# Kernel optimization log

Hardware: AMD Instinct MI355X
Metric: run time of the kernel (lower is better)

Reference implementation:

```python
import jax, jax.numpy as jnp
import numpy as np

B, C, H, W = 4, 128, 128, 128
G, K = 4, 3
P = K * K
STRIDE, PAD, DIL = 1, 1, 1
OFFSET_SCALE = 1.0


def setup_inputs() -> dict:
    key = jax.random.key(0)
    k1, k2, k3, k4 = jax.random.split(key, 4)
    inp = jax.random.normal(k1, (B, C, H, W), jnp.float32)
    # offset / mask linear params (zero-init in source; small random here for a
    # nontrivial sampling pattern -- same math, different param values)
    W_off = jax.random.normal(k2, (C, G * P * 2), jnp.float32) * 0.01
    b_off = jax.random.normal(k3, (G * P * 2,), jnp.float32) * 0.5
    W_mask = jax.random.normal(k4, (C, G * P), jnp.float32) * 0.02
    b_mask = jnp.zeros((G * P,), jnp.float32)
    return {"inp": inp, "W_off": W_off, "b_off": b_off, "W_mask": W_mask, "b_mask": b_mask}


def _dcnv3_core(x, offset, mask):
    # x: (b,h,w,c)  offset: (b,h,w,G*P*2)  mask: (b,h,w,G*P)
    b, h, w, c = x.shape
    gc = c // G
    xp = jnp.pad(x, ((0, 0), (PAD, PAD), (PAD, PAD), (0, 0)))
    H_in, W_in = h + 2 * PAD, w + 2 * PAD
    H_out = (H_in - (DIL * (K - 1) + 1)) // STRIDE + 1
    W_out = (W_in - (DIL * (K - 1) + 1)) // STRIDE + 1
    Q = H_out * W_out

    # reference points, normalized to padded size (matches _get_reference_points)
    base = (DIL * (K - 1)) // 2 + 0.5
    ref_y = (base + jnp.arange(H_out, dtype=jnp.float32) * STRIDE) / H_in
    ref_x = (base + jnp.arange(W_out, dtype=jnp.float32) * STRIDE) / W_in
    ref = jnp.stack(jnp.broadcast_arrays(ref_x[None, :], ref_y[:, None]), -1)  # (Ho,Wo,2) as (x,y)

    # dilation grid (matches _generate_dilation_grids; torch meshgrid flatten is x-major)
    off0 = -((DIL * (K - 1)) // 2)
    ks = off0 + jnp.arange(K, dtype=jnp.float32) * DIL
    gx = jnp.repeat(ks, K) / W_in  # (P,)
    gy = jnp.tile(ks, K) / H_in
    grid = jnp.stack([gx, gy], -1)  # (P,2), identical for every group

    norm = jnp.array([W_in, H_in], jnp.float32)
    loc = (ref[None, :, :, None, None, :]
           + grid[None, None, None, None, :, :] * OFFSET_SCALE
           + offset.reshape(b, H_out, W_out, G, P, 2) * (OFFSET_SCALE / norm))  # (b,Ho,Wo,G,P,2)

    # grid_sample(bilinear, zeros, align_corners=False): pixel = loc*size - 0.5
    px = loc[..., 0] * W_in - 0.5
    py = loc[..., 1] * H_in - 0.5
    x0 = jnp.floor(px); y0 = jnp.floor(py)
    tx = px - x0; ty = py - y0
    x0i = x0.astype(jnp.int32); y0i = y0.astype(jnp.int32)

    xg = xp.reshape(b, H_in * W_in, G, gc)

    def corner(ix, iy, wgt):
        valid = (ix >= 0) & (ix < W_in) & (iy >= 0) & (iy < H_in)
        lin = jnp.clip(iy, 0, H_in - 1) * W_in + jnp.clip(ix, 0, W_in - 1)
        idx = lin.reshape(b, Q, G, P).transpose(0, 1, 3, 2).reshape(b, Q * P, G)
        g = jnp.take_along_axis(xg, idx[..., None], axis=1)  # (b,Q*P,G,gc)
        wv = jnp.where(valid, wgt, 0.0).reshape(b, Q, G, P).transpose(0, 1, 3, 2).reshape(b, Q * P, G, 1)
        return g * wv

    val = (corner(x0i, y0i, (1 - tx) * (1 - ty))
           + corner(x0i + 1, y0i, tx * (1 - ty))
           + corner(x0i, y0i + 1, (1 - tx) * ty)
           + corner(x0i + 1, y0i + 1, tx * ty))  # (b,Q*P,G,gc)

    m = mask.reshape(b, Q, G, P).transpose(0, 1, 3, 2).reshape(b, Q, P, G, 1)
    out = (val.reshape(b, Q, P, G, gc) * m).sum(axis=2)  # (b,Q,G,gc)
    return out.reshape(b, H_out, W_out, G * gc)


def reference(inp, W_off, b_off, W_mask, b_mask):
    b, c, h, w = inp.shape
    x = inp.reshape(b, h, w, c)  # torch .view reinterpretation (faithful to source)
    offset = x @ W_off + b_off  # (b,h,w,G*P*2)
    mask = jax.nn.softmax((x @ W_mask + b_mask).reshape(b, h, w, G, P), axis=-1).reshape(b, h, w, G * P)
    out = _dcnv3_core(x, offset, mask)  # (b,h,w,c)
    return out.reshape(b, c, h, w)
```

## Files before the change

kernel.cpp:

```cpp
#include <hip/hip_runtime.h>


#define NPIX 65536

typedef unsigned int uint;
typedef unsigned short ushort;
typedef __attribute__((ext_vector_type(8))) short short8v;
typedef __attribute__((ext_vector_type(4))) float f32x4;

__device__ __forceinline__ ushort f2bf(float f) {
  uint u = __float_as_uint(f);
  u += 0x7FFFu + ((u >> 16) & 1u);
  return (ushort)(u >> 16);
}
__device__ __forceinline__ uint pkbf(float lo, float hi) {
  return (uint)f2bf(lo) | ((uint)f2bf(hi) << 16);
}
__device__ __forceinline__ float bflo(uint d) { return __uint_as_float(d << 16); }
__device__ __forceinline__ float bfhi(uint d) { return __uint_as_float(d & 0xFFFF0000u); }
__device__ __forceinline__ ushort f2h(float f) {
  union { _Float16 h; ushort u; } cv;
  cv.h = (_Float16)f;
  return cv.u;
}
__device__ __forceinline__ float h2f(ushort u) {
  union { ushort u; _Float16 h; } cv;
  cv.u = u;
  return (float)cv.h;
}

union U8 { uint u[4]; short8v v; };

__global__ __launch_bounds__(256) void dcn_lin_mfma(
    const float* __restrict__ x, const float* __restrict__ Woff,
    const float* __restrict__ boff, const float* __restrict__ Wmask,
    const float* __restrict__ bmask, ushort* __restrict__ ws16,
    ushort* __restrict__ x16) {
  __shared__ uint wt[112 * 68];
  __shared__ float bias_lds[112];
  const int pbase = blockIdx.x << 6;
  const int t = threadIdx.x;

  {
    int n = t, row = 0;
    bool act = true;
    if (t >= 224) act = false;
    else if (t >= 112) { n = t - 112; row = 1; }
    if (act) {
      for (int kp = row; kp < 64; kp += 2) {
        const int k = kp << 1;
        float w0, w1;
        if (n < 72) {
          w0 = Woff[k * 72 + n];        w1 = Woff[k * 72 + 72 + n];
        } else if (n < 108) {
          w0 = Wmask[k * 36 + n - 72];  w1 = Wmask[k * 36 + 36 + n - 72];
        } else {
          w0 = 0.f; w1 = 0.f;
        }
        wt[n * 68 + kp] = pkbf(w0, w1);
      }
    }
    if (t < 112)
      bias_lds[t] = (t < 72) ? boff[t] : (t < 108 ? bmask[t - 72] : 0.f);
  }

  if (x16) {
    const int pix2 = pbase + (t >> 2);
    const int quad = t & 3;
    const float* xp = x + (size_t)pix2 * 128 + (quad << 5);
    const int bb = pix2 >> 14, yx = pix2 & 16383;
    ushort* dst = x16 + ((((size_t)((quad << 2) | bb) << 14) | yx) << 5);
#pragma unroll
    for (int ck = 0; ck < 2; ++ck) {
      const float4 a = *(const float4*)(xp + ck * 16);
      const float4 b4 = *(const float4*)(xp + ck * 16 + 4);
      const float4 c4 = *(const float4*)(xp + ck * 16 + 8);
      const float4 d4 = *(const float4*)(xp + ck * 16 + 12);
      uint4 s0, s1;
      s0.x = pkbf(a.x, a.y);   s0.y = pkbf(a.z, a.w);
      s0.z = pkbf(b4.x, b4.y); s0.w = pkbf(b4.z, b4.w);
      s1.x = pkbf(c4.x, c4.y); s1.y = pkbf(c4.z, c4.w);
      s1.z = pkbf(d4.x, d4.y); s1.w = pkbf(d4.z, d4.w);
      *(uint4*)(dst + ck * 16) = s0;
      *(uint4*)(dst + ck * 16 + 8) = s1;
    }
  }
  __syncthreads();

  const int wv = t >> 6;
  const int lane = t & 63;
  const int lrow = lane & 15;
  const int lhi = lane >> 4;
  const int pixrow = pbase + (wv << 4) + lrow;

  U8 afr[4];
#pragma unroll
  for (int kt = 0; kt < 4; ++kt) {
    const float* ax = x + (size_t)pixrow * 128 + (kt << 5) + (lhi << 3);
    const float4 xa = *(const float4*)ax;
    const float4 xb4 = *(const float4*)(ax + 4);
    afr[kt].u[0] = pkbf(xa.x, xa.y);   afr[kt].u[1] = pkbf(xa.z, xa.w);
    afr[kt].u[2] = pkbf(xb4.x, xb4.y); afr[kt].u[3] = pkbf(xb4.z, xb4.w);
  }

  f32x4 acc[7];
#pragma unroll
  for (int nt = 0; nt < 7; ++nt) {
    const float bv = bias_lds[(nt << 4) + lrow];
    f32x4 a4 = {bv, bv, bv, bv};
#pragma unroll
    for (int kt = 0; kt < 4; ++kt) {
      U8 bfr;
      const uint4 bw =
          *(const uint4*)(wt + ((nt << 4) + lrow) * 68 + (kt << 4) + (lhi << 2));
      bfr.u[0] = bw.x; bfr.u[1] = bw.y; bfr.u[2] = bw.z; bfr.u[3] = bw.w;
      a4 = __builtin_amdgcn_mfma_f32_16x16x32_bf16(afr[kt].v, bfr.v, a4, 0, 0, 0);
    }
    acc[nt] = a4;
  }

  const int rowb = pbase + (wv << 4) + (lhi << 2);
#pragma unroll
  for (int nt = 0; nt < 7; ++nt) {
    const int n = (nt << 4) + lrow;
    if (n < 108) {
      ushort4 hv;
      hv.x = f2h(acc[nt].x);
      hv.y = f2h(acc[nt].y);
      hv.z = f2h(acc[nt].z);
      hv.w = f2h(acc[nt].w);
      *(ushort4*)(ws16 + (size_t)n * NPIX + rowb) = hv;
    }
  }
}

__global__ __launch_bounds__(256) void dcn_samp(
    const ushort* __restrict__ x16, const ushort* __restrict__ ws16,
    float* __restrict__ out) {
  const int g = blockIdx.x & 3;
  const int pg = threadIdx.x >> 2;
  const int sub = threadIdx.x & 3;
  const int q = ((blockIdx.x >> 2) << 6) | pg;
  const int b = q >> 14;
  const int h = (q >> 7) & 127;
  const int w = q & 127;
  const ushort* wsq = ws16 + q;
  const ushort* xg = x16 + (((size_t)((g << 2) | b)) << 19) + (sub << 3);

  float mk9[9];
  {
    float mx = -1e30f;
#pragma unroll
    for (int p = 0; p < 9; ++p) {
      mk9[p] = h2f(wsq[(size_t)(72 + g * 9 + p) * NPIX]);
      mx = fmaxf(mx, mk9[p]);
    }
    float s = 0.f;
#pragma unroll
    for (int p = 0; p < 9; ++p) {
      mk9[p] = __expf(mk9[p] - mx);
      s += mk9[p];
    }
    const float sinv = 1.0f / s;
#pragma unroll
    for (int p = 0; p < 9; ++p) mk9[p] *= sinv;
  }

  float a0 = 0.f, a1 = 0.f, a2 = 0.f, a3 = 0.f;
  float a4 = 0.f, a5 = 0.f, a6 = 0.f, a7 = 0.f;

#pragma unroll
  for (int p = 0; p < 9; ++p) {
    const float offx = h2f(wsq[(size_t)(g * 18 + 2 * p) * NPIX]);
    const float offy = h2f(wsq[(size_t)(g * 18 + 2 * p + 1) * NPIX]);
    const float mk = mk9[p];
    const float px = (float)(w + p / 3) + offx;
    const float py = (float)(h + p % 3) + offy;
    const float fx = floorf(px), fy = floorf(py);
    const float tx = px - fx, ty = py - fy;
    const int x0 = (int)fx - 1, y0 = (int)fy - 1;
    const int x1 = x0 + 1, y1 = y0 + 1;
    const float ax0 = ((unsigned)x0 < 128u) ? (1.f - tx) : 0.f;
    const float ax1 = ((unsigned)x1 < 128u) ? tx : 0.f;
    const float ay0 = ((unsigned)y0 < 128u) ? (mk * (1.f - ty)) : 0.f;
    const float ay1 = ((unsigned)y1 < 128u) ? (mk * ty) : 0.f;
    const float w00 = ax0 * ay0, w10 = ax1 * ay0;
    const float w01 = ax0 * ay1, w11 = ax1 * ay1;
    const int cx0 = min(max(x0, 0), 127), cy0 = min(max(y0, 0), 127);
    const int cx1 = min(max(x1, 0), 127), cy1 = min(max(y1, 0), 127);
    const int o00 = ((cy0 << 7) | cx0) << 5;
    const int o10 = ((cy0 << 7) | cx1) << 5;
    const int o01 = ((cy1 << 7) | cx0) << 5;
    const int o11 = ((cy1 << 7) | cx1) << 5;
    const uint4 d00 = *(const uint4*)(xg + o00);
    const uint4 d10 = *(const uint4*)(xg + o10);
    const uint4 d01 = *(const uint4*)(xg + o01);
    const uint4 d11 = *(const uint4*)(xg + o11);
    a0 = fmaf(w00, bflo(d00.x), fmaf(w10, bflo(d10.x),
         fmaf(w01, bflo(d01.x), fmaf(w11, bflo(d11.x), a0))));
    a1 = fmaf(w00, bfhi(d00.x), fmaf(w10, bfhi(d10.x),
         fmaf(w01, bfhi(d01.x), fmaf(w11, bfhi(d11.x), a1))));
    a2 = fmaf(w00, bflo(d00.y), fmaf(w10, bflo(d10.y),
         fmaf(w01, bflo(d01.y), fmaf(w11, bflo(d11.y), a2))));
    a3 = fmaf(w00, bfhi(d00.y), fmaf(w10, bfhi(d10.y),
         fmaf(w01, bfhi(d01.y), fmaf(w11, bfhi(d11.y), a3))));
    a4 = fmaf(w00, bflo(d00.z), fmaf(w10, bflo(d10.z),
         fmaf(w01, bflo(d01.z), fmaf(w11, bflo(d11.z), a4))));
    a5 = fmaf(w00, bfhi(d00.z), fmaf(w10, bfhi(d10.z),
         fmaf(w01, bfhi(d01.z), fmaf(w11, bfhi(d11.z), a5))));
    a6 = fmaf(w00, bflo(d00.w), fmaf(w10, bflo(d10.w),
         fmaf(w01, bflo(d01.w), fmaf(w11, bflo(d11.w), a6))));
    a7 = fmaf(w00, bfhi(d00.w), fmaf(w10, bfhi(d10.w),
         fmaf(w01, bfhi(d01.w), fmaf(w11, bfhi(d11.w), a7))));
  }

  float* op = out + (size_t)q * 128 + (g << 5) + (sub << 3);
  float4 oa, ob;
  oa.x = a0; oa.y = a1; oa.z = a2; oa.w = a3;
  ob.x = a4; ob.y = a5; ob.z = a6; ob.w = a7;
  *(float4*)op = oa;
  *(float4*)(op + 4) = ob;
}

__global__ __launch_bounds__(256) void dcn_lin(
    const float* __restrict__ x, const float* __restrict__ Woff,
    const float* __restrict__ boff, const float* __restrict__ Wmask,
    const float* __restrict__ bmask, float* __restrict__ ws) {
  const int jg = blockIdx.x >> 8;
  const int pix = ((blockIdx.x & 255) << 8) | threadIdx.x;
  const float* W;
  const float* bias;
  int ldw, obase;
  if (jg == 0) {
    W = Woff; bias = boff; ldw = 72; obase = 0;
  } else if (jg == 1) {
    W = Woff + 36; bias = boff + 36; ldw = 72; obase = 36;
  } else {
    W = Wmask; bias = bmask; ldw = 36; obase = 72;
  }
  float acc[36];
#pragma unroll
  for (int j = 0; j < 36; ++j) acc[j] = bias[j];
  const float* xp = x + (size_t)pix * 128;
  for (int c0 = 0; c0 < 128; c0 += 8) {
    float xr[8];
    *(float4*)(xr) = *(const float4*)(xp + c0);
    *(float4*)(xr + 4) = *(const float4*)(xp + c0 + 4);
#pragma unroll
    for (int cc = 0; cc < 8; ++cc) {
      const float xc = xr[cc];
      const float* wr = W + (size_t)(c0 + cc) * ldw;
#pragma unroll
      for (int j = 0; j < 36; ++j) acc[j] = fmaf(xc, wr[j], acc[j]);
    }
  }
  if (jg == 2) {
#pragma unroll
    for (int g = 0; g < 4; ++g) {
      float mx = acc[g * 9];
#pragma unroll
      for (int p = 1; p < 9; ++p) mx = fmaxf(mx, acc[g * 9 + p]);
      float s = 0.f;
#pragma unroll
      for (int p = 0; p < 9; ++p) {
        acc[g * 9 + p] = __expf(acc[g * 9 + p] - mx);
        s += acc[g * 9 + p];
      }
      const float sinv = 1.0f / s;
#pragma unroll
      for (int p = 0; p < 9; ++p) acc[g * 9 + p] *= sinv;
    }
  }
#pragma unroll
  for (int j = 0; j < 36; ++j) ws[(size_t)(obase + j) * NPIX + pix] = acc[j];
}

__global__ __launch_bounds__(256) void dcn_samp_f32(
    const float* __restrict__ x, const float* __restrict__ ws,
    float* __restrict__ out) {
  const int q = (blockIdx.x << 4) | (threadIdx.x >> 4);
  const int sub = threadIdx.x & 15;
  const int c = sub << 3;
  const int g = sub >> 2;
  const int b = q >> 14;
  const int h = (q >> 7) & 127;
  const int w = q & 127;
  const float* xb = x + ((size_t)b << 21) + c;
  const float* wsq = ws + q;
  float a0 = 0.f, a1 = 0.f, a2 = 0.f, a3 = 0.f;
  float a4 = 0.f, a5 = 0.f, a6 = 0.f, a7 = 0.f;
#pragma unroll
  for (int p = 0; p < 9; ++p) {
    const float offx = wsq[(size_t)(g * 18 + p * 2) * NPIX];
    const float offy = wsq[(size_t)(g * 18 + p * 2 + 1) * NPIX];
    const float mk = wsq[(size_t)(72 + g * 9 + p) * NPIX];
    const float px = (float)(w + p / 3) + offx;
    const float py = (float)(h + p % 3) + offy;
    const float fx = floorf(px), fy = floorf(py);
    const float tx = px - fx, ty = py - fy;
    const int x0 = (int)fx - 1, y0 = (int)fy - 1;
    const int x1 = x0 + 1, y1 = y0 + 1;
    const float ax0 = ((unsigned)x0 < 128u) ? (1.f - tx) : 0.f;
    const float ax1 = ((unsigned)x1 < 128u) ? tx : 0.f;
    const float ay0 = ((unsigned)y0 < 128u) ? (mk * (1.f - ty)) : 0.f;
    const float ay1 = ((unsigned)y1 < 128u) ? (mk * ty) : 0.f;
    const float w00 = ax0 * ay0, w10 = ax1 * ay0;
    const float w01 = ax0 * ay1, w11 = ax1 * ay1;
    const int cx0 = min(max(x0, 0), 127), cy0 = min(max(y0, 0), 127);
    const int cx1 = min(max(x1, 0), 127), cy1 = min(max(y1, 0), 127);
    const int o00 = (cy0 << 14) | (cx0 << 7), o10 = (cy0 << 14) | (cx1 << 7);
    const int o01 = (cy1 << 14) | (cx0 << 7), o11 = (cy1 << 14) | (cx1 << 7);
    const float4 v00a = *(const float4*)(xb + o00);
    const float4 v00b = *(const float4*)(xb + o00 + 4);
    const float4 v10a = *(const float4*)(xb + o10);
    const float4 v10b = *(const float4*)(xb + o10 + 4);
    const float4 v01a = *(const float4*)(xb + o01);
    const float4 v01b = *(const float4*)(xb + o01 + 4);
    const float4 v11a = *(const float4*)(xb + o11);
    const float4 v11b = *(const float4*)(xb + o11 + 4);
    a0 = fmaf(w00, v00a.x, fmaf(w10, v10a.x, fmaf(w01, v01a.x, fmaf(w11, v11a.x, a0))));
    a1 = fmaf(w00, v00a.y, fmaf(w10, v10a.y, fmaf(w01, v01a.y, fmaf(w11, v11a.y, a1))));
    a2 = fmaf(w00, v00a.z, fmaf(w10, v10a.z, fmaf(w01, v01a.z, fmaf(w11, v11a.z, a2))));
    a3 = fmaf(w00, v00a.w, fmaf(w10, v10a.w, fmaf(w01, v01a.w, fmaf(w11, v11a.w, a3))));
    a4 = fmaf(w00, v00b.x, fmaf(w10, v10b.x, fmaf(w01, v01b.x, fmaf(w11, v11b.x, a4))));
    a5 = fmaf(w00, v00b.y, fmaf(w10, v10b.y, fmaf(w01, v01b.y, fmaf(w11, v11b.y, a5))));
    a6 = fmaf(w00, v00b.z, fmaf(w10, v10b.z, fmaf(w01, v01b.z, fmaf(w11, v11b.z, a6))));
    a7 = fmaf(w00, v00b.w, fmaf(w10, v10b.w, fmaf(w01, v01b.w, fmaf(w11, v11b.w, a7))));
  }
  float4 oa, ob;
  oa.x = a0; oa.y = a1; oa.z = a2; oa.w = a3;
  ob.x = a4; ob.y = a5; ob.z = a6; ob.w = a7;
  float* op = out + (size_t)q * 128 + c;
  *(float4*)op = oa;
  *(float4*)(op + 4) = ob;
}

__global__ __launch_bounds__(128) void dcn_fused(
    const float* __restrict__ x, const float* __restrict__ Woff,
    const float* __restrict__ boff, const float* __restrict__ Wmask,
    const float* __restrict__ bmask, float* __restrict__ out) {
  __shared__ float xs[128];
  __shared__ float res[108];
  __shared__ float msk[36];
  const int q = blockIdx.x;
  const int t = threadIdx.x;
  const int b = q >> 14, h = (q >> 7) & 127, w = q & 127;
  xs[t] = x[(size_t)q * 128 + t];
  __syncthreads();
  if (t < 108) {
    float a;
    const float* W;
    int ld;
    if (t < 72) {
      a = boff[t]; W = Woff + t; ld = 72;
    } else {
      a = bmask[t - 72]; W = Wmask + (t - 72); ld = 36;
    }
    for (int cc = 0; cc < 128; ++cc) a = fmaf(xs[cc], W[(size_t)cc * ld], a);
    res[t] = a;
  }
  __syncthreads();
  if (t < 4) {
    float mx = -1e30f;
    for (int p = 0; p < 9; ++p) mx = fmaxf(mx, res[72 + t * 9 + p]);
    float s = 0.f;
    float e[9];
    for (int p = 0; p < 9; ++p) {
      e[p] = __expf(res[72 + t * 9 + p] - mx);
      s += e[p];
    }
    for (int p = 0; p < 9; ++p) msk[t * 9 + p] = e[p] / s;
  }
  __syncthreads();
  const int g = t >> 5;
  const float* xb = x + ((size_t)b << 21) + t;
  float acc = 0.f;
#pragma unroll
  for (int p = 0; p < 9; ++p) {
    const float offx = res[g * 18 + p * 2];
    const float offy = res[g * 18 + p * 2 + 1];
    const float px = (float)(w + p / 3) + offx;
    const float py = (float)(h + p % 3) + offy;
    const float fx = floorf(px), fy = floorf(py);
    const float tx = px - fx, ty = py - fy;
    const int x0 = (int)fx - 1, y0 = (int)fy - 1;
    float sv = 0.f;
#define CORNER1(XI, YI, WT)                                       \
  if ((unsigned)(XI) < 128u && (unsigned)(YI) < 128u)             \
    sv = fmaf((WT), xb[((size_t)(YI) << 14) + ((size_t)(XI) << 7)], sv);
    CORNER1(x0, y0, (1.f - tx) * (1.f - ty))
    CORNER1(x0 + 1, y0, tx * (1.f - ty))
    CORNER1(x0, y0 + 1, (1.f - tx) * ty)
    CORNER1(x0 + 1, y0 + 1, tx * ty)
#undef CORNER1
    acc = fmaf(msk[g * 9 + p], sv, acc);
  }
  out[(size_t)q * 128 + t] = acc;
}

extern "C" void kernel_launch(void* const* d_in, const int* in_sizes, int n_in,
                              void* d_out, int out_size, void* d_ws,
                              size_t ws_size, hipStream_t stream) {
  const float* x = (const float*)d_in[0];
  const float* Woff = (const float*)d_in[1];
  const float* boff = (const float*)d_in[2];
  const float* Wmask = (const float*)d_in[3];
  const float* bmask = (const float*)d_in[4];
  float* out = (float*)d_out;
  const size_t need_ws = (size_t)NPIX * 108 * sizeof(float);
  const size_t need_full = (size_t)NPIX * (128 + 108) * sizeof(ushort);
  if (ws_size >= need_full) {
    ushort* x16 = (ushort*)d_ws;
    ushort* ws16 = (ushort*)d_ws + (size_t)NPIX * 128;
    dcn_lin_mfma<<<1024, 256, 0, stream>>>(x, Woff, boff, Wmask, bmask, ws16,
                                           x16);
    dcn_samp<<<4096, 256, 0, stream>>>(x16, ws16, out);
  } else if (ws_size >= need_ws) {
    float* ws = (float*)d_ws;
    dcn_lin<<<768, 256, 0, stream>>>(x, Woff, boff, Wmask, bmask, ws);
    dcn_samp_f32<<<4096, 256, 0, stream>>>(x, ws, out);
  } else {
    dcn_fused<<<NPIX, 128, 0, stream>>>(x, Woff, boff, Wmask, bmask, out);
  }
}
```

Baseline: 62.05 us.

## Store offset/mask workspace pixel-major with per-group 32-half records

The linear kernel now transposes its MFMA results through LDS so that each pixel's offsets and masks are written as a contiguous 128-half record, padded to 32 halves per group. The sampling kernel then reads a group's 27 values with a few vector loads instead of 27 strided scalar loads spaced NPIX apart. This is meant to cut uncoalesced global reads in the sampler. In exchange it adds an LDS staging pass with extra barriers, and the workspace requirement grows slightly.

```diff
diff --git a/kernel.cpp b/kernel.cpp
--- a/kernel.cpp
+++ b/kernel.cpp
@@ -23,9 +23,14 @@
   cv.h = (_Float16)f;
   return cv.u;
 }
-__device__ __forceinline__ float h2f(ushort u) {
-  union { ushort u; _Float16 h; } cv;
-  cv.u = u;
+__device__ __forceinline__ float h2f_lo(uint u) {
+  union { ushort s; _Float16 h; } cv;
+  cv.s = (ushort)(u & 0xFFFFu);
+  return (float)cv.h;
+}
+__device__ __forceinline__ float h2f_hi(uint u) {
+  union { ushort s; _Float16 h; } cv;
+  cv.s = (ushort)(u >> 16);
   return (float)cv.h;
 }
 
@@ -119,17 +124,39 @@
     acc[nt] = a4;
   }
 
-  const int rowb = pbase + (wv << 4) + (lhi << 2);
-#pragma unroll
-  for (int nt = 0; nt < 7; ++nt) {
-    const int n = (nt << 4) + lrow;
-    if (n < 108) {
-      ushort4 hv;
-      hv.x = f2h(acc[nt].x);
-      hv.y = f2h(acc[nt].y);
-      hv.z = f2h(acc[nt].z);
-      hv.w = f2h(acc[nt].w);
-      *(ushort4*)(ws16 + (size_t)n * NPIX + rowb) = hv;
+  __syncthreads();
+  {
+    ushort* tl = (ushort*)wt;
+    const int plb = (wv << 4) + (lhi << 2);
+#pragma unroll
+    for (int nt = 0; nt < 7; ++nt) {
+      const int n = (nt << 4) + lrow;
+      if (n < 108) {
+        int ridx;
+        if (n < 72) {
+          const int gg = n / 18;
+          ridx = (gg << 5) + (n - gg * 18);
+        } else {
+          const int m = n - 72;
+          const int gg = m / 9;
+          ridx = (gg << 5) + 18 + (m - gg * 9);
+        }
+        tl[(plb + 0) * 128 + ridx] = f2h(acc[nt].x);
+        tl[(plb + 1) * 128 + ridx] = f2h(acc[nt].y);
+        tl[(plb + 2) * 128 + ridx] = f2h(acc[nt].z);
+        tl[(plb + 3) * 128 + ridx] = f2h(acc[nt].w);
+      }
+    }
+  }
+  __syncthreads();
+  {
+    const uint* src = (const uint*)wt;
+    uint4* dst = (uint4*)(ws16 + (size_t)pbase * 128);
+#pragma unroll
+    for (int i = 0; i < 4; ++i) {
+      const int idx = (i << 8) + t;
+      const uint4 v = *(const uint4*)(src + idx * 4);
+      dst[idx] = v;
     }
   }
 }
@@ -144,17 +171,32 @@
   const int b = q >> 14;
   const int h = (q >> 7) & 127;
   const int w = q & 127;
-  const ushort* wsq = ws16 + q;
   const ushort* xg = x16 + (((size_t)((g << 2) | b)) << 19) + (sub << 3);
 
-  float mk9[9];
+  const ushort* wsrec = ws16 + (size_t)q * 128 + (g << 5);
+  const uint4 r0 = *(const uint4*)(wsrec);
+  const uint4 r1 = *(const uint4*)(wsrec + 8);
+  const uint4 r2 = *(const uint4*)(wsrec + 16);
+  const uint2 r3 = *(const uint2*)(wsrec + 24);
+  const uint rr0 = r0.x, rr1 = r0.y, rr2 = r0.z, rr3 = r0.w;
+  const uint rr4 = r1.x, rr5 = r1.y, rr6 = r1.z, rr7 = r1.w;
+  const uint rr8 = r2.x, rr9 = r2.y, rr10 = r2.z, rr11 = r2.w;
+  const uint rr12 = r3.x, rr13 = r3.y;
+
+  float offx9[9], offy9[9], mk9[9];
   {
-    float mx = -1e30f;
+    const uint rra[14] = {rr0, rr1, rr2,  rr3,  rr4,  rr5,  rr6,
+                          rr7, rr8, rr9, rr10, rr11, rr12, rr13};
 #pragma unroll
     for (int p = 0; p < 9; ++p) {
-      mk9[p] = h2f(wsq[(size_t)(72 + g * 9 + p) * NPIX]);
-      mx = fmaxf(mx, mk9[p]);
-    }
+      offx9[p] = h2f_lo(rra[p]);
+      offy9[p] = h2f_hi(rra[p]);
+      const int li = 18 + p;
+      mk9[p] = (li & 1) ? h2f_hi(rra[li >> 1]) : h2f_lo(rra[li >> 1]);
+    }
+    float mx = mk9[0];
+#pragma unroll
+    for (int p = 1; p < 9; ++p) mx = fmaxf(mx, mk9[p]);
     float s = 0.f;
 #pragma unroll
     for (int p = 0; p < 9; ++p) {
@@ -171,11 +213,9 @@
 
 #pragma unroll
   for (int p = 0; p < 9; ++p) {
-    const float offx = h2f(wsq[(size_t)(g * 18 + 2 * p) * NPIX]);
-    const float offy = h2f(wsq[(size_t)(g * 18 + 2 * p + 1) * NPIX]);
     const float mk = mk9[p];
-    const float px = (float)(w + p / 3) + offx;
-    const float py = (float)(h + p % 3) + offy;
+    const float px = (float)(w + p / 3) + offx9[p];
+    const float py = (float)(h + p % 3) + offy9[p];
     const float fx = floorf(px), fy = floorf(py);
     const float tx = px - fx, ty = py - fy;
     const int x0 = (int)fx - 1, y0 = (int)fy - 1;
@@ -408,7 +448,7 @@
   const float* bmask = (const float*)d_in[4];
   float* out = (float*)d_out;
   const size_t need_ws = (size_t)NPIX * 108 * sizeof(float);
-  const size_t need_full = (size_t)NPIX * (128 + 108) * sizeof(ushort);
+  const size_t need_full = (size_t)NPIX * (128 + 128) * sizeof(ushort);
   if (ws_size >= need_full) {
     ushort* x16 = (ushort*)d_ws;
     ushort* ws16 = (ushort*)d_ws + (size_t)NPIX * 128;
```

After: 60.87 us. About the same (-1.9%).
